# Kernel optimization log

Measured on AMD Instinct MI355X. Metric: run time of the kernel, lower is better.

Reference implementation:

```python
import jax, jax.numpy as jnp
import numpy as np
import math

D_MODEL = 1024
N_HEADS = 16
HEAD_DIM = D_MODEL // N_HEADS
THETA = 10000.0


def _rope(x, cos, sin):
    # x: [b, h, s, head_dim]; cos/sin: [s, head_dim//2]
    xe = x[..., 0::2]
    xo = x[..., 1::2]
    re = xe * cos - xo * sin
    ro = xe * sin + xo * cos
    # interleave back to even/odd layout
    return jnp.stack([re, ro], axis=-1).reshape(x.shape)


def setup_inputs() -> dict:
    key = jax.random.key(0)
    k1, k2, k3, k4, k5 = jax.random.split(key, 5)
    std = math.sqrt(2.0 / (D_MODEL + D_MODEL))
    x = jax.random.normal(k1, (2, 2048, D_MODEL), dtype=jnp.float32)
    Wq = jax.random.normal(k2, (D_MODEL, D_MODEL), dtype=jnp.float32) * std
    Wk = jax.random.normal(k3, (D_MODEL, D_MODEL), dtype=jnp.float32) * std
    Wv = jax.random.normal(k4, (D_MODEL, D_MODEL), dtype=jnp.float32) * std
    Wo = jax.random.normal(k5, (D_MODEL, D_MODEL), dtype=jnp.float32) * (std / math.sqrt(2))
    return {"x": x, "Wq": Wq, "Wk": Wk, "Wv": Wv, "Wo": Wo}


def reference(x, Wq, Wk, Wv, Wo):
    b, s, d = x.shape
    h, hd = N_HEADS, HEAD_DIM
    # projections: einsum 'batch seq d_in, d_model d_in -> batch seq d_model' == x @ W.T
    def proj(W):
        y = jnp.einsum('bsd,md->bsm', x, W)
        return y.reshape(b, s, h, hd).transpose(0, 2, 1, 3)  # [b, h, s, hd]
    Q, K, V = proj(Wq), proj(Wk), proj(Wv)
    # RoPE with default positions = arange(seq)
    freqs = 1.0 / (THETA ** (jnp.arange(0, hd, 2, dtype=jnp.float32) / hd))
    angles = jnp.arange(s, dtype=jnp.float32)[:, None] * freqs[None, :]  # [s, hd//2]
    cos, sin = jnp.cos(angles), jnp.sin(angles)
    Q = _rope(Q, cos, sin)
    K = _rope(K, cos, sin)
    # naive causal attention
    scores = jnp.einsum('bhqd,bhkd->bhqk', Q, K) / math.sqrt(hd)
    causal = jnp.tril(jnp.ones((s, s), dtype=bool))
    scores = jnp.where(causal, scores, -jnp.inf)
    attn = jax.nn.softmax(scores, axis=-1)
    out = jnp.einsum('bhqk,bhkd->bhqd', attn, V)
    out = out.transpose(0, 2, 1, 3).reshape(b, s, d)
    return jnp.einsum('bsd,md->bsm', out, Wo)
```

## Files before the change

### kernel.cpp

```cpp
#include <hip/hip_runtime.h>
#include <stdint.h>
#include <stddef.h>

typedef __bf16 bf16;
typedef __bf16 bf16x8 __attribute__((ext_vector_type(8)));
typedef __bf16 bf16x4 __attribute__((ext_vector_type(4)));
typedef short short4v __attribute__((ext_vector_type(4)));
typedef float f32x4 __attribute__((ext_vector_type(4)));

#define GAS __attribute__((address_space(1)))
#define LAS __attribute__((address_space(3)))

__device__ __forceinline__ void async_load16(const void* g, void* l) {
  __builtin_amdgcn_global_load_lds((const GAS void*)g, (LAS void*)l, 16, 0, 0);
}

__device__ __forceinline__ f32x4 mfma16(bf16x4 a, bf16x4 b, f32x4 c) {
#if defined(__HIP_DEVICE_COMPILE__)
#if __has_builtin(__builtin_amdgcn_mfma_f32_16x16x16bf16_1k)
  return __builtin_amdgcn_mfma_f32_16x16x16bf16_1k(
      __builtin_bit_cast(short4v, a), __builtin_bit_cast(short4v, b), c, 0, 0, 0);
#else
  f32x4 d;
  asm volatile("v_mfma_f32_16x16x16_bf16 %0, %1, %2, %3"
               : "=v"(d)
               : "v"(a), "v"(b), "v"(c));
  return d;
#endif
#else
  (void)a; (void)b;
  return c;
#endif
}

__global__ __launch_bounds__(256) void cast_all(
    const float* __restrict__ x, const float* __restrict__ Wq,
    const float* __restrict__ Wk, const float* __restrict__ Wv,
    const float* __restrict__ Wo, bf16* __restrict__ Xh,
    bf16* __restrict__ Wqkv, bf16* __restrict__ Woh) {
  int idx = blockIdx.x * 256 + threadIdx.x;
  if (idx < 4194304) {
    Xh[idx] = (bf16)x[idx];
  } else if (idx < 7340032) {
    int j = idx - 4194304;
    if (j < 1048576) {
      Wqkv[j] = (bf16)(Wq[j] * 0.18033688011112042f);
    } else {
      const float* W = (j < 2097152) ? Wk : Wv;
      Wqkv[j] = (bf16)W[j & 1048575];
    }
  } else {
    int j = idx - 7340032;
    Woh[j] = (bf16)Wo[j];
  }
}

__global__ __launch_bounds__(256) void gemm_qkv(
    const bf16* __restrict__ A, const bf16* __restrict__ B,
    bf16* __restrict__ QKV2, bf16* __restrict__ Vt, int K) {
  __shared__ __align__(16) bf16 As[128 * 32];
  __shared__ __align__(16) bf16 Bs[128 * 32];
  const int tid = threadIdx.x;
  const int wave = tid >> 6, lane = tid & 63;
  const int bm = blockIdx.y * 128, bn = blockIdx.x * 128;
  const int wm = (wave >> 1) * 64, wn = (wave & 1) * 64;
  const int lrow = lane >> 2, lk = (lane & 3) * 8;
  const int fr = lane & 15, fk = (lane >> 4) * 8;

  f32x4 acc[4][4] = {};

  for (int kt = 0; kt < K; kt += 32) {
    __syncthreads();
#pragma unroll
    for (int c = 0; c < 2; ++c) {
      const int chunk = wave * 2 + c;
      const bf16* ga = A + (size_t)(bm + chunk * 16 + lrow) * K + kt + lk;
      async_load16(ga, (void*)(As + chunk * 512));
      const bf16* gb = B + (size_t)(bn + chunk * 16 + lrow) * K + kt + lk;
      async_load16(gb, (void*)(Bs + chunk * 512));
    }
    __syncthreads();

    bf16x8 af[4], bfr[4];
#pragma unroll
    for (int i = 0; i < 4; ++i)
      af[i] = *(const bf16x8*)&As[(wm + i * 16 + fr) * 32 + fk];
#pragma unroll
    for (int j = 0; j < 4; ++j)
      bfr[j] = *(const bf16x8*)&Bs[(wn + j * 16 + fr) * 32 + fk];
#pragma unroll
    for (int i = 0; i < 4; ++i)
#pragma unroll
      for (int j = 0; j < 4; ++j)
        acc[i][j] =
            __builtin_amdgcn_mfma_f32_16x16x32_bf16(af[i], bfr[j], acc[i][j], 0, 0, 0);
  }

  const int r0 = (lane >> 4) * 4, cc = lane & 15;
#pragma unroll
  for (int i = 0; i < 4; ++i) {
    const int row0 = bm + wm + i * 16 + r0;
#pragma unroll
    for (int j = 0; j < 4; ++j) {
      const int col = bn + wn + j * 16 + cc;
      if (col < 2048) {
#pragma unroll
        for (int r = 0; r < 4; ++r)
          QKV2[(size_t)(row0 + r) * 2048 + col] = (bf16)acc[i][j][r];
      } else {
        const int v = col - 2048, h = v >> 6, d = v & 63;
        const int b = row0 >> 11, s = row0 & 2047;
        bf16x4 o;
#pragma unroll
        for (int r = 0; r < 4; ++r) o[r] = (bf16)acc[i][j][r];
        *(bf16x4*)&Vt[(((size_t)b * 16 + h) * 64 + d) * 2048 + s] = o;
      }
    }
  }
}

template <typename OutT, int BM, int BN>
__global__ __launch_bounds__(256) void gemm_bt(
    const bf16* __restrict__ A, const bf16* __restrict__ B,
    OutT* __restrict__ C, int M, int N, int K) {
  constexpr int ACH = BM / 16, NCH = (BM + BN) / 16, PW = NCH / 4;
  constexpr int FM = BM / 32, FN = BN / 32;
  __shared__ __align__(16) bf16 As[BM * 32];
  __shared__ __align__(16) bf16 Bs[BN * 32];
  const int tid = threadIdx.x;
  const int wave = tid >> 6, lane = tid & 63;
  const int bm = blockIdx.y * BM, bn = blockIdx.x * BN;
  const int wm = (wave >> 1) * (BM / 2), wn = (wave & 1) * (BN / 2);
  const int lrow = lane >> 2, lk = (lane & 3) * 8;
  const int fr = lane & 15, fk = (lane >> 4) * 8;

  f32x4 acc[FM][FN] = {};

  for (int kt = 0; kt < K; kt += 32) {
    __syncthreads();
#pragma unroll
    for (int c = 0; c < PW; ++c) {
      const int chunk = wave * PW + c;
      if (chunk < ACH) {
        const bf16* ga = A + (size_t)(bm + chunk * 16 + lrow) * K + kt + lk;
        async_load16(ga, (void*)(As + chunk * 512));
      } else {
        const int bc = chunk - ACH;
        const bf16* gb = B + (size_t)(bn + bc * 16 + lrow) * K + kt + lk;
        async_load16(gb, (void*)(Bs + bc * 512));
      }
    }
    __syncthreads();

    bf16x8 af[FM], bfr[FN];
#pragma unroll
    for (int i = 0; i < FM; ++i)
      af[i] = *(const bf16x8*)&As[(wm + i * 16 + fr) * 32 + fk];
#pragma unroll
    for (int j = 0; j < FN; ++j)
      bfr[j] = *(const bf16x8*)&Bs[(wn + j * 16 + fr) * 32 + fk];
#pragma unroll
    for (int i = 0; i < FM; ++i)
#pragma unroll
      for (int j = 0; j < FN; ++j)
        acc[i][j] =
            __builtin_amdgcn_mfma_f32_16x16x32_bf16(af[i], bfr[j], acc[i][j], 0, 0, 0);
  }

  const int r0 = (lane >> 4) * 4, cc = lane & 15;
#pragma unroll
  for (int i = 0; i < FM; ++i)
#pragma unroll
    for (int j = 0; j < FN; ++j)
#pragma unroll
      for (int r = 0; r < 4; ++r)
        C[(size_t)(bm + wm + i * 16 + r0 + r) * N + (bn + wn + j * 16 + cc)] =
            (OutT)acc[i][j][r];
}

__global__ __launch_bounds__(256) void rope_qk(const bf16* __restrict__ QKV2,
                                               bf16* __restrict__ Qh,
                                               bf16* __restrict__ Kh) {
  int idx = blockIdx.x * 256 + threadIdx.x;
  int row = idx >> 10, cp = idx & 1023;
  int col = cp << 1;
  size_t base = (size_t)row * 2048 + col;
  float xe = (float)QKV2[base], xo = (float)QKV2[base + 1];
  int s = row & 2047, b = row >> 11;
  int i = cp & 31;
  float freq = __expf((float)i * -0.2878231366242557f);
  float sn, cs;
  __sincosf((float)s * freq, &sn, &cs);
  float re = xe * cs - xo * sn;
  float ro = xe * sn + xo * cs;
  int hcol = col & 1023;
  int h = hcol >> 6, d = hcol & 63;
  bf16* dst = (col < 1024 ? Qh : Kh) + ((size_t)(b * 16 + h) * 2048 + s) * 64 + d;
  dst[0] = (bf16)re;
  dst[1] = (bf16)ro;
}

__global__ __launch_bounds__(128, 2) void attn(const bf16* __restrict__ Qh,
                                               const bf16* __restrict__ Kh,
                                               const bf16* __restrict__ Vt,
                                               bf16* __restrict__ Oh) {
  __shared__ __align__(16) bf16 Vs[2][64 * 72];
  __shared__ float scratch[68 * 64];
  const int f = blockIdx.x;
  const int qt = 31 - (f >> 5);
  const int bh = f & 31;
  const int tid = threadIdx.x, w = tid >> 6, lane = tid & 63;
  const int nlo = lane & 15, g = lane >> 4;
  const int q0 = qt * 64;
  const bf16* __restrict__ Qp = Qh + (size_t)bh * 131072;
  const bf16* __restrict__ Kp = Kh + (size_t)bh * 131072;
  const bf16* __restrict__ Vp = Vt + (size_t)bh * 131072;
  const int n = qt + 1;
  const int hf = (n + 1) >> 1;
  const int t0 = w ? hf : 0;
  const int cnt = w ? (n - hf) : hf;

  bf16x8 aq[4][2];
#pragma unroll
  for (int qb = 0; qb < 4; ++qb)
#pragma unroll
    for (int ks = 0; ks < 2; ++ks)
      aq[qb][ks] =
          *(const bf16x8*)&Qp[(size_t)(q0 + qb * 16 + nlo) * 64 + ks * 32 + g * 8];

  f32x4 oacc[4][4] = {};
  float lsum[4] = {0.f, 0.f, 0.f, 0.f};

  const int srow = lane >> 3, soff = (lane & 7) * 8;
  bf16* __restrict__ Vw = Vs[w];

  bf16x8 pv[8];
  if (cnt > 0) {
#pragma unroll
    for (int c = 0; c < 8; ++c)
      pv[c] = *(const bf16x8*)&Vp[(size_t)(c * 8 + srow) * 2048 + t0 * 64 + soff];
  }

  for (int it = 0; it < cnt; ++it) {
    const int i = t0 + it, kbase = i * 64;
    bf16x8 pk[4][2];
#pragma unroll
    for (int ni = 0; ni < 4; ++ni)
#pragma unroll
      for (int ks = 0; ks < 2; ++ks)
        pk[ni][ks] = *(const bf16x8*)&Kp[(size_t)(kbase + ni * 16 + nlo) * 64 +
                                         ks * 32 + g * 8];
#pragma unroll
    for (int c = 0; c < 8; ++c)
      *(bf16x8*)&Vw[(c * 8 + srow) * 72 + soff] = pv[c];
    if (it + 1 < cnt) {
      const int kb2 = kbase + 64;
#pragma unroll
      for (int c = 0; c < 8; ++c)
        pv[c] = *(const bf16x8*)&Vp[(size_t)(c * 8 + srow) * 2048 + kb2 + soff];
    }

    const bool dg = (i == n - 1);
    bf16x4 p[4][4];
#pragma unroll
    for (int qb = 0; qb < 4; ++qb) {
      f32x4 st[4] = {};
#pragma unroll
      for (int ks = 0; ks < 2; ++ks)
#pragma unroll
        for (int ni = 0; ni < 4; ++ni)
          st[ni] = __builtin_amdgcn_mfma_f32_16x16x32_bf16(pk[ni][ks], aq[qb][ks],
                                                           st[ni], 0, 0, 0);
      const int qg = q0 + qb * 16 + nlo;
#pragma unroll
      for (int ni = 0; ni < 4; ++ni) {
        const int kg0 = kbase + ni * 16 + g * 4;
#pragma unroll
        for (int r = 0; r < 4; ++r) {
          float e = __builtin_amdgcn_exp2f(st[ni][r]);
          e = (!dg || (kg0 + r <= qg)) ? e : 0.0f;
          lsum[qb] += e;
          p[qb][ni][r] = (bf16)e;
        }
      }
    }

#pragma unroll
    for (int ni = 0; ni < 4; ++ni)
#pragma unroll
      for (int mi = 0; mi < 4; ++mi) {
        bf16x4 av = *(const bf16x4*)&Vw[(mi * 16 + nlo) * 72 + ni * 16 + g * 4];
#pragma unroll
        for (int qb = 0; qb < 4; ++qb)
          oacc[qb][mi] = mfma16(av, p[qb][ni], oacc[qb][mi]);
      }
  }

#pragma unroll
  for (int qb = 0; qb < 4; ++qb) {
    lsum[qb] += __shfl_xor(lsum[qb], 16, 64);
    lsum[qb] += __shfl_xor(lsum[qb], 32, 64);
  }

  if (w == 1) {
#pragma unroll
    for (int qb = 0; qb < 4; ++qb) {
#pragma unroll
      for (int mi = 0; mi < 4; ++mi)
#pragma unroll
        for (int r = 0; r < 4; ++r)
          scratch[(qb * 16 + mi * 4 + r) * 64 + lane] = oacc[qb][mi][r];
      scratch[(64 + qb) * 64 + lane] = lsum[qb];
    }
  }
  __syncthreads();
  if (w == 0) {
    const int b = bh >> 4, hd = bh & 15;
#pragma unroll
    for (int qb = 0; qb < 4; ++qb) {
      const float l = lsum[qb] + scratch[(64 + qb) * 64 + lane];
      const float inv = 1.0f / l;
      const int q = q0 + qb * 16 + nlo;
#pragma unroll
      for (int mi = 0; mi < 4; ++mi) {
        bf16x4 o;
#pragma unroll
        for (int r = 0; r < 4; ++r)
          o[r] = (bf16)((oacc[qb][mi][r] +
                         scratch[(qb * 16 + mi * 4 + r) * 64 + lane]) * inv);
        *(bf16x4*)&Oh[((size_t)b * 2048 + q) * 1024 + hd * 64 + mi * 16 + g * 4] = o;
      }
    }
  }
}

extern "C" void kernel_launch(void* const* d_in, const int* in_sizes, int n_in,
                              void* d_out, int out_size, void* d_ws, size_t ws_size,
                              hipStream_t stream) {
  (void)in_sizes; (void)n_in; (void)out_size; (void)ws_size;
  const float* x = (const float*)d_in[0];
  const float* Wq = (const float*)d_in[1];
  const float* Wk = (const float*)d_in[2];
  const float* Wv = (const float*)d_in[3];
  const float* Wo = (const float*)d_in[4];
  float* out = (float*)d_out;
  char* ws = (char*)d_ws;

  bf16* Xh   = (bf16*)(ws);
  bf16* Wqkv = (bf16*)(ws + 8388608);
  bf16* Woh  = (bf16*)(ws + 14680064);
  bf16* QKV2 = (bf16*)(ws + 16777216);
  bf16* Qh   = (bf16*)(ws + 33554432);
  bf16* Kh   = (bf16*)(ws + 41943040);
  bf16* Vt   = (bf16*)(ws + 50331648);
  bf16* Oh   = (bf16*)(ws + 58720256);

  cast_all<<<32768, 256, 0, stream>>>(x, Wq, Wk, Wv, Wo, Xh, Wqkv, Woh);
  gemm_qkv<<<dim3(24, 32), 256, 0, stream>>>(Xh, Wqkv, QKV2, Vt, 1024);
  rope_qk<<<16384, 256, 0, stream>>>(QKV2, Qh, Kh);
  attn<<<1024, 128, 0, stream>>>(Qh, Kh, Vt, Oh);
  gemm_bt<float, 128, 64><<<dim3(16, 32), 256, 0, stream>>>(Oh, Woh, out, 4096, 1024, 1024);
}
```

Measured before the change: 204.5 us.

## Split attention KV range across four waves per block with tree reduction

The attention kernel now runs four waves per query tile instead of two. Each wave processes a quarter of the causal KV tiles, and the partial outputs and row sums are combined through shared memory in two reduction stages. The grid becomes 2D with q-tile on x and head on y, which changes block scheduling order, and the launch bounds go to 256 threads with 4 blocks per CU. This aims for more parallelism per query tile and shorter per-wave serial chains. In exchange it adds reduction traffic, extra barriers and register-pressure limits.

```diff
diff --git a/kernel.cpp b/kernel.cpp
--- a/kernel.cpp
+++ b/kernel.cpp
@@ -200,15 +200,13 @@
   dst[1] = (bf16)ro;
 }
 
-__global__ __launch_bounds__(128, 2) void attn(const bf16* __restrict__ Qh,
+__global__ __launch_bounds__(256, 4) void attn(const bf16* __restrict__ Qh,
                                                const bf16* __restrict__ Kh,
                                                const bf16* __restrict__ Vt,
                                                bf16* __restrict__ Oh) {
-  __shared__ __align__(16) bf16 Vs[2][64 * 72];
-  __shared__ float scratch[68 * 64];
-  const int f = blockIdx.x;
-  const int qt = 31 - (f >> 5);
-  const int bh = f & 31;
+  __shared__ __align__(16) char smem[4 * 64 * 72 * 2];
+  const int qt = 31 - (int)blockIdx.x;
+  const int bh = blockIdx.y;
   const int tid = threadIdx.x, w = tid >> 6, lane = tid & 63;
   const int nlo = lane & 15, g = lane >> 4;
   const int q0 = qt * 64;
@@ -216,9 +214,8 @@
   const bf16* __restrict__ Kp = Kh + (size_t)bh * 131072;
   const bf16* __restrict__ Vp = Vt + (size_t)bh * 131072;
   const int n = qt + 1;
-  const int hf = (n + 1) >> 1;
-  const int t0 = w ? hf : 0;
-  const int cnt = w ? (n - hf) : hf;
+  const int t0 = (n * w) >> 2, t1 = (n * (w + 1)) >> 2;
+  const int cnt = t1 - t0;
 
   bf16x8 aq[4][2];
 #pragma unroll
@@ -232,7 +229,7 @@
   float lsum[4] = {0.f, 0.f, 0.f, 0.f};
 
   const int srow = lane >> 3, soff = (lane & 7) * 8;
-  bf16* __restrict__ Vw = Vs[w];
+  bf16* __restrict__ Vw = (bf16*)smem + w * 4608;
 
   bf16x8 pv[8];
   if (cnt > 0) {
@@ -302,15 +299,44 @@
     lsum[qb] += __shfl_xor(lsum[qb], 32, 64);
   }
 
-  if (w == 1) {
+  float* sc0 = (float*)smem;
+  float* sc1 = (float*)smem + 4352;
+  __syncthreads();
+  if (w == 1 || w == 3) {
+    float* sc = (w == 1) ? sc0 : sc1;
 #pragma unroll
     for (int qb = 0; qb < 4; ++qb) {
 #pragma unroll
       for (int mi = 0; mi < 4; ++mi)
 #pragma unroll
         for (int r = 0; r < 4; ++r)
-          scratch[(qb * 16 + mi * 4 + r) * 64 + lane] = oacc[qb][mi][r];
-      scratch[(64 + qb) * 64 + lane] = lsum[qb];
+          sc[(qb * 16 + mi * 4 + r) * 64 + lane] = oacc[qb][mi][r];
+      sc[(64 + qb) * 64 + lane] = lsum[qb];
+    }
+  }
+  __syncthreads();
+  if (w == 0) {
+#pragma unroll
+    for (int qb = 0; qb < 4; ++qb) {
+#pragma unroll
+      for (int mi = 0; mi < 4; ++mi)
+#pragma unroll
+        for (int r = 0; r < 4; ++r)
+          oacc[qb][mi][r] += sc0[(qb * 16 + mi * 4 + r) * 64 + lane] +
+                             sc1[(qb * 16 + mi * 4 + r) * 64 + lane];
+      lsum[qb] += sc0[(64 + qb) * 64 + lane] + sc1[(64 + qb) * 64 + lane];
+    }
+  }
+  __syncthreads();
+  if (w == 2) {
+#pragma unroll
+    for (int qb = 0; qb < 4; ++qb) {
+#pragma unroll
+      for (int mi = 0; mi < 4; ++mi)
+#pragma unroll
+        for (int r = 0; r < 4; ++r)
+          sc0[(qb * 16 + mi * 4 + r) * 64 + lane] = oacc[qb][mi][r];
+      sc0[(64 + qb) * 64 + lane] = lsum[qb];
     }
   }
   __syncthreads();
@@ -318,7 +344,7 @@
     const int b = bh >> 4, hd = bh & 15;
 #pragma unroll
     for (int qb = 0; qb < 4; ++qb) {
-      const float l = lsum[qb] + scratch[(64 + qb) * 64 + lane];
+      const float l = lsum[qb] + sc0[(64 + qb) * 64 + lane];
       const float inv = 1.0f / l;
       const int q = q0 + qb * 16 + nlo;
 #pragma unroll
@@ -327,7 +353,7 @@
 #pragma unroll
         for (int r = 0; r < 4; ++r)
           o[r] = (bf16)((oacc[qb][mi][r] +
-                         scratch[(qb * 16 + mi * 4 + r) * 64 + lane]) * inv);
+                         sc0[(qb * 16 + mi * 4 + r) * 64 + lane]) * inv);
         *(bf16x4*)&Oh[((size_t)b * 2048 + q) * 1024 + hd * 64 + mi * 16 + g * 4] = o;
       }
     }
@@ -358,6 +384,6 @@
   cast_all<<<32768, 256, 0, stream>>>(x, Wq, Wk, Wv, Wo, Xh, Wqkv, Woh);
   gemm_qkv<<<dim3(24, 32), 256, 0, stream>>>(Xh, Wqkv, QKV2, Vt, 1024);
   rope_qk<<<16384, 256, 0, stream>>>(QKV2, Qh, Kh);
-  attn<<<1024, 128, 0, stream>>>(Qh, Kh, Vt, Oh);
+  attn<<<dim3(32, 32), 256, 0, stream>>>(Qh, Kh, Vt, Oh);
   gemm_bt<float, 128, 64><<<dim3(16, 32), 256, 0, stream>>>(Oh, Woh, out, 4096, 1024, 1024);
 }
```

Result: slower. 398.9 us, median of 2 (+95.1%).
